# Kernel optimization log

Measured on AMD Instinct MI355X. Metric: run time of the kernel, lower is better.

The kernel has to match this reference:

```python
import jax, jax.numpy as jnp
import numpy as np


def _gcn_prep(edge_index, num_nodes):
    # GCNConv default: remove nothing, add self loops, symmetric normalization
    self_loops = jnp.arange(num_nodes, dtype=edge_index.dtype)
    row = jnp.concatenate([edge_index[0], self_loops])  # source j
    col = jnp.concatenate([edge_index[1], self_loops])  # target i
    deg = jax.ops.segment_sum(jnp.ones_like(col, dtype=jnp.float32), col,
                              num_segments=num_nodes)
    dinv = jnp.where(deg > 0, jax.lax.rsqrt(deg), 0.0)
    norm = dinv[row] * dinv[col]  # [E + N]
    return row, col, norm


def _gcn_conv(x, row, col, norm, W, b):
    # linear transform first (smaller feature dim kept), then gather-scale-scatter
    h = x @ W                               # [N, out]
    msg = h[row] * norm[:, None]            # [E+N, out] gather (irregular access)
    out = jax.ops.segment_sum(msg, col, num_segments=x.shape[0])
    return out + b


def setup_inputs() -> dict:
    key = jax.random.key(0)
    k1, k2, k3, k4, k5 = jax.random.split(key, 5)
    N, F, H, C, E = 50000, 128, 128, 64, 800000
    x = jax.random.normal(k1, (N, F), dtype=jnp.float32)
    edge_index = jax.random.randint(k2, (2, E), 0, N, dtype=jnp.int64)
    # Glorot-ish initialized GCN layer parameters
    W1 = jax.random.normal(k3, (F, H), dtype=jnp.float32) * (1.0 / np.sqrt(F))
    b1 = jnp.zeros((H,), dtype=jnp.float32)
    W2 = jax.random.normal(k4, (H, C), dtype=jnp.float32) * (1.0 / np.sqrt(H))
    b2 = jnp.zeros((C,), dtype=jnp.float32)
    return {"x": x, "edge_index": edge_index, "W1": W1, "b1": b1,
            "W2": W2, "b2": b2}


def reference(x, edge_index, W1, b1, W2, b2):
    # eval-mode forward: dropout(p=0 / eval) is identity
    N = x.shape[0]
    row, col, norm = _gcn_prep(edge_index, N)
    h = _gcn_conv(x, row, col, norm, W1, b1)   # conv1
    h = jax.nn.elu(h)                          # F.elu
    out = _gcn_conv(h, row, col, norm, W2, b2) # conv2
    return out
```

## Files before the change

### kernel.cpp

```cpp
#include <hip/hip_runtime.h>
#include <hip/hip_bf16.h>
#include <math.h>


typedef short bf16x8 __attribute__((ext_vector_type(8)));
typedef float f32x4  __attribute__((ext_vector_type(4)));

#define BCAP 6144
#define CCAP 64

__device__ __forceinline__ unsigned short bf16rne(float f) {
    unsigned u = __float_as_uint(f);
    unsigned r = u + 0x7FFFu + ((u >> 16) & 1u);
    return (unsigned short)(r >> 16);
}
__device__ __forceinline__ float bf16tof(unsigned short h) {
    return __uint_as_float(((unsigned)h) << 16);
}
__device__ __forceinline__ void split2(float v, unsigned short& hi, unsigned short& lo) {
    hi = bf16rne(v);
    lo = bf16rne(v - bf16tof(hi));
}
__device__ __forceinline__ float lo16f(unsigned u) { return __uint_as_float(u << 16); }
__device__ __forceinline__ float hi16f(unsigned u) { return __uint_as_float(u & 0xFFFF0000u); }

__device__ __forceinline__ f32x4 mfma_bf16(bf16x8 a, bf16x8 b, f32x4 c) {
    return __builtin_amdgcn_mfma_f32_16x16x32_bf16(a, b, c, 0, 0, 0);
}

__device__ __forceinline__ int detect64(const int* __restrict__ ei) {
    return (ei[1] | ei[3] | ei[5] | ei[7] | ei[9] | ei[11] | ei[13] | ei[15]) == 0;
}
__device__ __forceinline__ int edge_row(const int* ei, long long E, int is64, int e) {
    return is64 ? ei[2 * (long long)e] : ei[e];
}
__device__ __forceinline__ int edge_col(const int* ei, long long E, int is64, int e) {
    return is64 ? ei[2 * (E + (long long)e)] : ei[E + e];
}

__global__ __launch_bounds__(256) void k_cvt(const float* __restrict__ x,
                                             unsigned short* __restrict__ xhi,
                                             unsigned short* __restrict__ xlo, int total4,
                                             const float* __restrict__ W1,
                                             const float* __restrict__ W2,
                                             unsigned short* __restrict__ w1hi,
                                             unsigned short* __restrict__ w1lo,
                                             unsigned short* __restrict__ w2hi,
                                             unsigned short* __restrict__ w2lo,
                                             int n1, int n2, int H, int C, int nbCvtX) {
    int bid = blockIdx.x;
    if (bid < nbCvtX) {
        int t = bid * 256 + threadIdx.x;
        if (t >= total4) return;
        float4 v = reinterpret_cast<const float4*>(x)[t];
        unsigned short h0, h1, h2, h3, l0, l1, l2, l3;
        split2(v.x, h0, l0); split2(v.y, h1, l1);
        split2(v.z, h2, l2); split2(v.w, h3, l3);
        unsigned long long hp = (unsigned long long)h0 | ((unsigned long long)h1 << 16) |
                                ((unsigned long long)h2 << 32) | ((unsigned long long)h3 << 48);
        unsigned long long lp = (unsigned long long)l0 | ((unsigned long long)l1 << 16) |
                                ((unsigned long long)l2 << 32) | ((unsigned long long)l3 << 48);
        reinterpret_cast<unsigned long long*>(xhi)[t] = hp;
        reinterpret_cast<unsigned long long*>(xlo)[t] = lp;
        return;
    }
    bid -= nbCvtX;
    int t = bid * 256 + threadIdx.x;
    unsigned short h, l;
    if (t < n1) {
        int k = t / H, n = t % H;
        split2(W1[t], h, l);
        w1hi[n * 128 + k] = h;
        w1lo[n * 128 + k] = l;
    } else if (t < n1 + n2) {
        int q = t - n1;
        int k = q / C, n = q % C;
        split2(W2[q], h, l);
        w2hi[n * 128 + k] = h;
        w2lo[n * 128 + k] = l;
    }
}

__global__ __launch_bounds__(256) void k_bucket(const int* __restrict__ ei, int E,
                                                int* __restrict__ bcur,
                                                unsigned* __restrict__ ebuf, int N) {
    __shared__ int lcnt[256];
    __shared__ int lbase[256];
    int t = threadIdx.x;
    lcnt[t] = 0;
    __syncthreads();
    int is64 = detect64(ei);
    int e0 = blockIdx.x * 2048;
    int loff[8], bb[8];
    unsigned pk[8];
    bool val[8];
    #pragma unroll
    for (int k = 0; k < 8; ++k) {
        int e = e0 + k * 256 + t;
        val[k] = (e < E);
        int c = val[k] ? edge_col(ei, E, is64, e) : 0;
        int r = val[k] ? edge_row(ei, E, is64, e) : 0;
        bb[k] = c >> 8;
        pk[k] = ((unsigned)r << 16) | (unsigned)(c & 255);
        loff[k] = val[k] ? atomicAdd(&lcnt[bb[k]], 1) : 0;
    }
    __syncthreads();
    int nbk = (N + 255) >> 8;
    if (t < nbk && lcnt[t] > 0) lbase[t] = atomicAdd(&bcur[t], lcnt[t]);
    __syncthreads();
    #pragma unroll
    for (int k = 0; k < 8; ++k) {
        if (!val[k]) continue;
        int p = lbase[bb[k]] + loff[k];
        if (p < BCAP) ebuf[(size_t)bb[k] * BCAP + p] = pk[k];
    }
}

__global__ __launch_bounds__(256) void k_fine(const unsigned* __restrict__ ebuf,
                                              const int* __restrict__ bcur,
                                              unsigned short* __restrict__ csrc,
                                              int* __restrict__ cnt,
                                              float* __restrict__ dinv, int N) {
    __shared__ int cur[256];
    __shared__ unsigned short slots[256 * CCAP];
    int t = threadIdx.x;
    cur[t] = 0;
    __syncthreads();
    int b = blockIdx.x;
    int cb = bcur[b];
    cb = (cb < BCAP) ? cb : BCAP;
    const unsigned* src = ebuf + (size_t)b * BCAP;
    for (int i = t; i < cb; i += 256) {
        unsigned v = src[i];
        int local = v & 255;
        int pos = atomicAdd(&cur[local], 1);
        if (pos < CCAP) slots[(local << 6) + pos] = (unsigned short)(v >> 16);
    }
    __syncthreads();
    int n0 = b << 8;
    int n = n0 + t;
    if (n < N) {
        int c = cur[t];
        cnt[n] = (c < CCAP) ? c : CCAP;
        dinv[n] = 1.0f / sqrtf((float)(c + 1));
    }
    const unsigned* s32 = reinterpret_cast<const unsigned*>(slots);
    unsigned* d32 = reinterpret_cast<unsigned*>(csrc);
    #pragma unroll
    for (int r = 0; r < 32; ++r) {
        int idx = r * 256 + t;
        int node = idx >> 5, m = idx & 31;
        int gn = n0 + node;
        if (gn < N) d32[(size_t)gn * 32 + m] = s32[(node << 5) + m];
    }
}

template <int NOUT>
__global__ __launch_bounds__(256) void k_gemm_mfma(const unsigned short* __restrict__ Ahi,
                                                   const unsigned short* __restrict__ Alo,
                                                   const unsigned short* __restrict__ BThi,
                                                   const unsigned short* __restrict__ BTlo,
                                                   const float* __restrict__ dinv,
                                                   unsigned short* __restrict__ Cb, int N) {
    constexpr int NT = NOUT / 16;
    int wid = threadIdx.x >> 6, lane = threadIdx.x & 63;
    int row0 = blockIdx.x * 128 + wid * 32;
    int ml = lane & 15, kg = lane >> 4;

    f32x4 acc[2][NT] = {};

    int r0 = row0 + ml, r1 = row0 + 16 + ml;
    int ar0 = (r0 < N) ? r0 : (N - 1);
    int ar1 = (r1 < N) ? r1 : (N - 1);

    for (int kt = 0; kt < 4; ++kt) {
        int k0 = kt * 32 + kg * 8;
        bf16x8 a0h = *reinterpret_cast<const bf16x8*>(&Ahi[(size_t)ar0 * 128 + k0]);
        bf16x8 a0l = *reinterpret_cast<const bf16x8*>(&Alo[(size_t)ar0 * 128 + k0]);
        bf16x8 a1h = *reinterpret_cast<const bf16x8*>(&Ahi[(size_t)ar1 * 128 + k0]);
        bf16x8 a1l = *reinterpret_cast<const bf16x8*>(&Alo[(size_t)ar1 * 128 + k0]);
        #pragma unroll
        for (int nt = 0; nt < NT; ++nt) {
            bf16x8 bh = *reinterpret_cast<const bf16x8*>(&BThi[(size_t)(nt * 16 + ml) * 128 + k0]);
            bf16x8 bl = *reinterpret_cast<const bf16x8*>(&BTlo[(size_t)(nt * 16 + ml) * 128 + k0]);
            acc[0][nt] = mfma_bf16(a0h, bh, acc[0][nt]);
            acc[0][nt] = mfma_bf16(a0l, bh, acc[0][nt]);
            acc[0][nt] = mfma_bf16(a0h, bl, acc[0][nt]);
            acc[1][nt] = mfma_bf16(a1h, bh, acc[1][nt]);
            acc[1][nt] = mfma_bf16(a1l, bh, acc[1][nt]);
            acc[1][nt] = mfma_bf16(a1h, bl, acc[1][nt]);
        }
    }

    #pragma unroll
    for (int rt = 0; rt < 2; ++rt) {
        #pragma unroll
        for (int r = 0; r < 4; ++r) {
            int row = row0 + rt * 16 + kg * 4 + r;
            if (row < N) {
                float d = dinv[row];
                #pragma unroll
                for (int nt = 0; nt < NT; ++nt)
                    Cb[(size_t)row * NOUT + nt * 16 + ml] = bf16rne(acc[rt][nt][r] * d);
            }
        }
    }
}

__global__ __launch_bounds__(256) void k_agg1(const unsigned* __restrict__ hb,
                                              const unsigned short* __restrict__ csr,
                                              const int* __restrict__ cnt,
                                              const float* __restrict__ dinv,
                                              const float* __restrict__ bias,
                                              unsigned* __restrict__ yhi,
                                              unsigned* __restrict__ ylo, int N) {
    int wid  = (blockIdx.x * 256 + threadIdx.x) >> 6;
    int lane = threadIdx.x & 63;
    if (wid >= N) return;
    int i = wid;
    unsigned us = hb[(size_t)i * 64 + lane];
    float ax0 = lo16f(us), ay0 = hi16f(us);
    float ax1 = 0.f, ay1 = 0.f, ax2 = 0.f, ay2 = 0.f, ax3 = 0.f, ay3 = 0.f;
    float ax4 = 0.f, ay4 = 0.f, ax5 = 0.f, ay5 = 0.f, ax6 = 0.f, ay6 = 0.f;
    float ax7 = 0.f, ay7 = 0.f;
    int c = cnt[i];
    int s = i << 6, e = s + c;
    int p = s;
    for (; p + 8 <= e; p += 8) {
        int j0 = csr[p + 0], j1 = csr[p + 1], j2 = csr[p + 2], j3 = csr[p + 3];
        int j4 = csr[p + 4], j5 = csr[p + 5], j6 = csr[p + 6], j7 = csr[p + 7];
        unsigned u0 = hb[(size_t)j0 * 64 + lane];
        unsigned u1 = hb[(size_t)j1 * 64 + lane];
        unsigned u2 = hb[(size_t)j2 * 64 + lane];
        unsigned u3 = hb[(size_t)j3 * 64 + lane];
        unsigned u4 = hb[(size_t)j4 * 64 + lane];
        unsigned u5 = hb[(size_t)j5 * 64 + lane];
        unsigned u6 = hb[(size_t)j6 * 64 + lane];
        unsigned u7 = hb[(size_t)j7 * 64 + lane];
        ax0 += lo16f(u0); ay0 += hi16f(u0);  ax1 += lo16f(u1); ay1 += hi16f(u1);
        ax2 += lo16f(u2); ay2 += hi16f(u2);  ax3 += lo16f(u3); ay3 += hi16f(u3);
        ax4 += lo16f(u4); ay4 += hi16f(u4);  ax5 += lo16f(u5); ay5 += hi16f(u5);
        ax6 += lo16f(u6); ay6 += hi16f(u6);  ax7 += lo16f(u7); ay7 += hi16f(u7);
    }
    if (p + 4 <= e) {
        int j0 = csr[p + 0], j1 = csr[p + 1], j2 = csr[p + 2], j3 = csr[p + 3];
        unsigned u0 = hb[(size_t)j0 * 64 + lane];
        unsigned u1 = hb[(size_t)j1 * 64 + lane];
        unsigned u2 = hb[(size_t)j2 * 64 + lane];
        unsigned u3 = hb[(size_t)j3 * 64 + lane];
        ax0 += lo16f(u0); ay0 += hi16f(u0);  ax1 += lo16f(u1); ay1 += hi16f(u1);
        ax2 += lo16f(u2); ay2 += hi16f(u2);  ax3 += lo16f(u3); ay3 += hi16f(u3);
        p += 4;
    }
    for (; p < e; ++p) {
        unsigned u = hb[(size_t)csr[p] * 64 + lane];
        ax0 += lo16f(u); ay0 += hi16f(u);
    }
    float sx = (ax0 + ax1) + (ax2 + ax3) + (ax4 + ax5) + (ax6 + ax7);
    float sy = (ay0 + ay1) + (ay2 + ay3) + (ay4 + ay5) + (ay6 + ay7);
    float di = dinv[i];
    float2 bb = reinterpret_cast<const float2*>(bias)[lane];
    float vx = di * sx + bb.x;
    float vy = di * sy + bb.y;
    vx = vx > 0.f ? vx : (expf(vx) - 1.f);
    vy = vy > 0.f ? vy : (expf(vy) - 1.f);
    unsigned short hx, lx, hy, ly;
    split2(vx, hx, lx);
    split2(vy, hy, ly);
    yhi[(size_t)i * 64 + lane] = (unsigned)hx | ((unsigned)hy << 16);
    ylo[(size_t)i * 64 + lane] = (unsigned)lx | ((unsigned)ly << 16);
}

__global__ __launch_bounds__(256) void k_agg2(const unsigned short* __restrict__ hb,
                                              const unsigned short* __restrict__ csr,
                                              const int* __restrict__ cnt,
                                              const float* __restrict__ dinv,
                                              const float* __restrict__ bias,
                                              float* __restrict__ out, int N) {
    int wid  = (blockIdx.x * 256 + threadIdx.x) >> 6;
    int lane = threadIdx.x & 63;
    if (wid >= N) return;
    int i = wid;
    float a0 = bf16tof(hb[(size_t)i * 64 + lane]);
    float a1 = 0.f, a2 = 0.f, a3 = 0.f, a4 = 0.f, a5 = 0.f, a6 = 0.f, a7 = 0.f;
    int c = cnt[i];
    int s = i << 6, e = s + c;
    int p = s;
    for (; p + 8 <= e; p += 8) {
        int j0 = csr[p + 0], j1 = csr[p + 1], j2 = csr[p + 2], j3 = csr[p + 3];
        int j4 = csr[p + 4], j5 = csr[p + 5], j6 = csr[p + 6], j7 = csr[p + 7];
        a0 += bf16tof(hb[(size_t)j0 * 64 + lane]);
        a1 += bf16tof(hb[(size_t)j1 * 64 + lane]);
        a2 += bf16tof(hb[(size_t)j2 * 64 + lane]);
        a3 += bf16tof(hb[(size_t)j3 * 64 + lane]);
        a4 += bf16tof(hb[(size_t)j4 * 64 + lane]);
        a5 += bf16tof(hb[(size_t)j5 * 64 + lane]);
        a6 += bf16tof(hb[(size_t)j6 * 64 + lane]);
        a7 += bf16tof(hb[(size_t)j7 * 64 + lane]);
    }
    if (p + 4 <= e) {
        a0 += bf16tof(hb[(size_t)csr[p + 0] * 64 + lane]);
        a1 += bf16tof(hb[(size_t)csr[p + 1] * 64 + lane]);
        a2 += bf16tof(hb[(size_t)csr[p + 2] * 64 + lane]);
        a3 += bf16tof(hb[(size_t)csr[p + 3] * 64 + lane]);
        p += 4;
    }
    for (; p < e; ++p) a0 += bf16tof(hb[(size_t)csr[p] * 64 + lane]);
    float sum = (a0 + a1) + (a2 + a3) + (a4 + a5) + (a6 + a7);
    out[(size_t)i * 64 + lane] = dinv[i] * sum + bias[lane];
}

extern "C" void kernel_launch(void* const* d_in, const int* in_sizes, int n_in,
                              void* d_out, int out_size, void* d_ws, size_t ws_size,
                              hipStream_t stream) {
    const float* x  = (const float*)d_in[0];
    const int*   ei = (const int*)d_in[1];
    const float* W1 = (const float*)d_in[2];
    const float* b1 = (const float*)d_in[3];
    const float* W2 = (const float*)d_in[4];
    const float* b2 = (const float*)d_in[5];

    const int H = in_sizes[3];
    const int C = in_sizes[5];
    const int F = in_sizes[2] / H;
    const int N = in_sizes[0] / F;
    const int E = in_sizes[1] / 2;
    float* out = (float*)d_out;

    char* w = (char*)d_ws;
    auto alloc = [&](size_t bytes) -> char* {
        char* p = w;
        w += (bytes + 255) & ~(size_t)255;
        return p;
    };
    const int nbB = (N + 255) >> 8;
    int*   bcur  = (int*)alloc((size_t)nbB * sizeof(int));
    int*   cnt   = (int*)alloc((size_t)N * sizeof(int));
    float* dinv  = (float*)alloc((size_t)N * sizeof(float));
    unsigned* ebuf = (unsigned*)alloc((size_t)nbB * BCAP * sizeof(unsigned));
    unsigned short* csrc = (unsigned short*)alloc((size_t)N * CCAP * 2);
    unsigned short* xhi  = (unsigned short*)alloc((size_t)N * F * 2);
    unsigned short* xlo  = (unsigned short*)alloc((size_t)N * F * 2);
    unsigned short* w1hi = (unsigned short*)alloc((size_t)F * H * 2);
    unsigned short* w1lo = (unsigned short*)alloc((size_t)F * H * 2);
    unsigned short* w2hi = (unsigned short*)alloc((size_t)H * C * 2);
    unsigned short* w2lo = (unsigned short*)alloc((size_t)H * C * 2);
    unsigned short* h1b  = (unsigned short*)alloc((size_t)N * H * 2);
    unsigned*       y1hi = (unsigned*)alloc((size_t)N * H * 2);
    unsigned*       y1lo = (unsigned*)alloc((size_t)N * H * 2);
    unsigned short* h2b  = (unsigned short*)alloc((size_t)N * C * 2);

    const int total4  = N * F / 4;
    const int nbCvtX  = (total4 + 255) / 256;
    const int nbCvtW  = (F * H + H * C + 255) / 256;
    const int nbAgg   = (N + 3) / 4;

    hipMemsetAsync(bcur, 0, (size_t)nbB * sizeof(int), stream);
    k_bucket<<<(E + 2047) / 2048, 256, 0, stream>>>(ei, E, bcur, ebuf, N);
    k_fine<<<nbB, 256, 0, stream>>>(ebuf, bcur, csrc, cnt, dinv, N);
    k_cvt<<<nbCvtX + nbCvtW, 256, 0, stream>>>(x, xhi, xlo, total4, W1, W2,
                                               w1hi, w1lo, w2hi, w2lo,
                                               F * H, H * C, H, C, nbCvtX);

    k_gemm_mfma<128><<<(N + 127) / 128, 256, 0, stream>>>(xhi, xlo, w1hi, w1lo, dinv, h1b, N);
    k_agg1<<<nbAgg, 256, 0, stream>>>(
        reinterpret_cast<const unsigned*>(h1b), csrc, cnt, dinv, b1, y1hi, y1lo, N);
    k_gemm_mfma<64><<<(N + 127) / 128, 256, 0, stream>>>(
        (const unsigned short*)y1hi, (const unsigned short*)y1lo, w2hi, w2lo, dinv, h2b, N);
    k_agg2<<<nbAgg, 256, 0, stream>>>(h2b, csrc, cnt, dinv, b2, out, N);
}
```

Measured before the change: 144.2 us.

## Fuse x bf16 splitting into GEMM and store layer-2 input as single bf16

Removes the standalone x conversion pass by splitting fp32 x into bf16 hi/lo inside the first GEMM's operand load, eliminating the hi/lo intermediate buffers. The aggregated ELU output now stores only a single bf16 value, and the second GEMM skips the low-part MFMA. This cuts global memory traffic and MFMA work, at the cost of reduced precision for the second layer's input.

```diff
diff --git a/kernel.cpp b/kernel.cpp
--- a/kernel.cpp
+++ b/kernel.cpp
@@ -38,34 +38,14 @@
     return is64 ? ei[2 * (E + (long long)e)] : ei[E + e];
 }
 
-__global__ __launch_bounds__(256) void k_cvt(const float* __restrict__ x,
-                                             unsigned short* __restrict__ xhi,
-                                             unsigned short* __restrict__ xlo, int total4,
-                                             const float* __restrict__ W1,
-                                             const float* __restrict__ W2,
-                                             unsigned short* __restrict__ w1hi,
-                                             unsigned short* __restrict__ w1lo,
-                                             unsigned short* __restrict__ w2hi,
-                                             unsigned short* __restrict__ w2lo,
-                                             int n1, int n2, int H, int C, int nbCvtX) {
-    int bid = blockIdx.x;
-    if (bid < nbCvtX) {
-        int t = bid * 256 + threadIdx.x;
-        if (t >= total4) return;
-        float4 v = reinterpret_cast<const float4*>(x)[t];
-        unsigned short h0, h1, h2, h3, l0, l1, l2, l3;
-        split2(v.x, h0, l0); split2(v.y, h1, l1);
-        split2(v.z, h2, l2); split2(v.w, h3, l3);
-        unsigned long long hp = (unsigned long long)h0 | ((unsigned long long)h1 << 16) |
-                                ((unsigned long long)h2 << 32) | ((unsigned long long)h3 << 48);
-        unsigned long long lp = (unsigned long long)l0 | ((unsigned long long)l1 << 16) |
-                                ((unsigned long long)l2 << 32) | ((unsigned long long)l3 << 48);
-        reinterpret_cast<unsigned long long*>(xhi)[t] = hp;
-        reinterpret_cast<unsigned long long*>(xlo)[t] = lp;
-        return;
-    }
-    bid -= nbCvtX;
-    int t = bid * 256 + threadIdx.x;
+__global__ __launch_bounds__(256) void k_cvtw(const float* __restrict__ W1,
+                                              const float* __restrict__ W2,
+                                              unsigned short* __restrict__ w1hi,
+                                              unsigned short* __restrict__ w1lo,
+                                              unsigned short* __restrict__ w2hi,
+                                              unsigned short* __restrict__ w2lo,
+                                              int n1, int n2, int H, int C) {
+    int t = blockIdx.x * 256 + threadIdx.x;
     unsigned short h, l;
     if (t < n1) {
         int k = t / H, n = t % H;
@@ -155,9 +135,9 @@
     }
 }
 
-template <int NOUT>
-__global__ __launch_bounds__(256) void k_gemm_mfma(const unsigned short* __restrict__ Ahi,
-                                                   const unsigned short* __restrict__ Alo,
+template <int NOUT, bool AF32>
+__global__ __launch_bounds__(256) void k_gemm_mfma(const float* __restrict__ Af,
+                                                   const unsigned short* __restrict__ Ab,
                                                    const unsigned short* __restrict__ BThi,
                                                    const unsigned short* __restrict__ BTlo,
                                                    const float* __restrict__ dinv,
@@ -175,20 +155,45 @@
 
     for (int kt = 0; kt < 4; ++kt) {
         int k0 = kt * 32 + kg * 8;
-        bf16x8 a0h = *reinterpret_cast<const bf16x8*>(&Ahi[(size_t)ar0 * 128 + k0]);
-        bf16x8 a0l = *reinterpret_cast<const bf16x8*>(&Alo[(size_t)ar0 * 128 + k0]);
-        bf16x8 a1h = *reinterpret_cast<const bf16x8*>(&Ahi[(size_t)ar1 * 128 + k0]);
-        bf16x8 a1l = *reinterpret_cast<const bf16x8*>(&Alo[(size_t)ar1 * 128 + k0]);
+        bf16x8 a0h, a0l, a1h, a1l;
+        if constexpr (AF32) {
+            float4 v0 = *reinterpret_cast<const float4*>(&Af[(size_t)ar0 * 128 + k0]);
+            float4 v1 = *reinterpret_cast<const float4*>(&Af[(size_t)ar0 * 128 + k0 + 4]);
+            float4 v2 = *reinterpret_cast<const float4*>(&Af[(size_t)ar1 * 128 + k0]);
+            float4 v3 = *reinterpret_cast<const float4*>(&Af[(size_t)ar1 * 128 + k0 + 4]);
+            unsigned short h, l;
+            split2(v0.x, h, l); a0h[0] = (short)h; a0l[0] = (short)l;
+            split2(v0.y, h, l); a0h[1] = (short)h; a0l[1] = (short)l;
+            split2(v0.z, h, l); a0h[2] = (short)h; a0l[2] = (short)l;
+            split2(v0.w, h, l); a0h[3] = (short)h; a0l[3] = (short)l;
+            split2(v1.x, h, l); a0h[4] = (short)h; a0l[4] = (short)l;
+            split2(v1.y, h, l); a0h[5] = (short)h; a0l[5] = (short)l;
+            split2(v1.z, h, l); a0h[6] = (short)h; a0l[6] = (short)l;
+            split2(v1.w, h, l); a0h[7] = (short)h; a0l[7] = (short)l;
+            split2(v2.x, h, l); a1h[0] = (short)h; a1l[0] = (short)l;
+            split2(v2.y, h, l); a1h[1] = (short)h; a1l[1] = (short)l;
+            split2(v2.z, h, l); a1h[2] = (short)h; a1l[2] = (short)l;
+            split2(v2.w, h, l); a1h[3] = (short)h; a1l[3] = (short)l;
+            split2(v3.x, h, l); a1h[4] = (short)h; a1l[4] = (short)l;
+            split2(v3.y, h, l); a1h[5] = (short)h; a1l[5] = (short)l;
+            split2(v3.z, h, l); a1h[6] = (short)h; a1l[6] = (short)l;
+            split2(v3.w, h, l); a1h[7] = (short)h; a1l[7] = (short)l;
+        } else {
+            a0h = *reinterpret_cast<const bf16x8*>(&Ab[(size_t)ar0 * 128 + k0]);
+            a1h = *reinterpret_cast<const bf16x8*>(&Ab[(size_t)ar1 * 128 + k0]);
+        }
         #pragma unroll
         for (int nt = 0; nt < NT; ++nt) {
             bf16x8 bh = *reinterpret_cast<const bf16x8*>(&BThi[(size_t)(nt * 16 + ml) * 128 + k0]);
             bf16x8 bl = *reinterpret_cast<const bf16x8*>(&BTlo[(size_t)(nt * 16 + ml) * 128 + k0]);
             acc[0][nt] = mfma_bf16(a0h, bh, acc[0][nt]);
-            acc[0][nt] = mfma_bf16(a0l, bh, acc[0][nt]);
             acc[0][nt] = mfma_bf16(a0h, bl, acc[0][nt]);
             acc[1][nt] = mfma_bf16(a1h, bh, acc[1][nt]);
-            acc[1][nt] = mfma_bf16(a1l, bh, acc[1][nt]);
             acc[1][nt] = mfma_bf16(a1h, bl, acc[1][nt]);
+            if constexpr (AF32) {
+                acc[0][nt] = mfma_bf16(a0l, bh, acc[0][nt]);
+                acc[1][nt] = mfma_bf16(a1l, bh, acc[1][nt]);
+            }
         }
     }
 
@@ -212,8 +217,7 @@
                                               const int* __restrict__ cnt,
                                               const float* __restrict__ dinv,
                                               const float* __restrict__ bias,
-                                              unsigned* __restrict__ yhi,
-                                              unsigned* __restrict__ ylo, int N) {
+                                              unsigned* __restrict__ y1b, int N) {
     int wid  = (blockIdx.x * 256 + threadIdx.x) >> 6;
     int lane = threadIdx.x & 63;
     if (wid >= N) return;
@@ -264,11 +268,7 @@
     float vy = di * sy + bb.y;
     vx = vx > 0.f ? vx : (expf(vx) - 1.f);
     vy = vy > 0.f ? vy : (expf(vy) - 1.f);
-    unsigned short hx, lx, hy, ly;
-    split2(vx, hx, lx);
-    split2(vy, hy, ly);
-    yhi[(size_t)i * 64 + lane] = (unsigned)hx | ((unsigned)hy << 16);
-    ylo[(size_t)i * 64 + lane] = (unsigned)lx | ((unsigned)ly << 16);
+    y1b[(size_t)i * 64 + lane] = (unsigned)bf16rne(vx) | ((unsigned)bf16rne(vy) << 16);
 }
 
 __global__ __launch_bounds__(256) void k_agg2(const unsigned short* __restrict__ hb,
@@ -339,33 +339,27 @@
     float* dinv  = (float*)alloc((size_t)N * sizeof(float));
     unsigned* ebuf = (unsigned*)alloc((size_t)nbB * BCAP * sizeof(unsigned));
     unsigned short* csrc = (unsigned short*)alloc((size_t)N * CCAP * 2);
-    unsigned short* xhi  = (unsigned short*)alloc((size_t)N * F * 2);
-    unsigned short* xlo  = (unsigned short*)alloc((size_t)N * F * 2);
     unsigned short* w1hi = (unsigned short*)alloc((size_t)F * H * 2);
     unsigned short* w1lo = (unsigned short*)alloc((size_t)F * H * 2);
     unsigned short* w2hi = (unsigned short*)alloc((size_t)H * C * 2);
     unsigned short* w2lo = (unsigned short*)alloc((size_t)H * C * 2);
     unsigned short* h1b  = (unsigned short*)alloc((size_t)N * H * 2);
-    unsigned*       y1hi = (unsigned*)alloc((size_t)N * H * 2);
-    unsigned*       y1lo = (unsigned*)alloc((size_t)N * H * 2);
+    unsigned*       y1b  = (unsigned*)alloc((size_t)N * H * 2);
     unsigned short* h2b  = (unsigned short*)alloc((size_t)N * C * 2);
 
-    const int total4  = N * F / 4;
-    const int nbCvtX  = (total4 + 255) / 256;
-    const int nbCvtW  = (F * H + H * C + 255) / 256;
-    const int nbAgg   = (N + 3) / 4;
+    const int nbAgg = (N + 3) / 4;
 
     hipMemsetAsync(bcur, 0, (size_t)nbB * sizeof(int), stream);
     k_bucket<<<(E + 2047) / 2048, 256, 0, stream>>>(ei, E, bcur, ebuf, N);
     k_fine<<<nbB, 256, 0, stream>>>(ebuf, bcur, csrc, cnt, dinv, N);
-    k_cvt<<<nbCvtX + nbCvtW, 256, 0, stream>>>(x, xhi, xlo, total4, W1, W2,
-                                               w1hi, w1lo, w2hi, w2lo,
-                                               F * H, H * C, H, C, nbCvtX);
-
-    k_gemm_mfma<128><<<(N + 127) / 128, 256, 0, stream>>>(xhi, xlo, w1hi, w1lo, dinv, h1b, N);
+    k_cvtw<<<(F * H + H * C + 255) / 256, 256, 0, stream>>>(W1, W2, w1hi, w1lo, w2hi, w2lo,
+                                                            F * H, H * C, H, C);
+
+    k_gemm_mfma<128, true><<<(N + 127) / 128, 256, 0, stream>>>(
+        x, nullptr, w1hi, w1lo, dinv, h1b, N);
     k_agg1<<<nbAgg, 256, 0, stream>>>(
-        reinterpret_cast<const unsigned*>(h1b), csrc, cnt, dinv, b1, y1hi, y1lo, N);
-    k_gemm_mfma<64><<<(N + 127) / 128, 256, 0, stream>>>(
-        (const unsigned short*)y1hi, (const unsigned short*)y1lo, w2hi, w2lo, dinv, h2b, N);
+        reinterpret_cast<const unsigned*>(h1b), csrc, cnt, dinv, b1, y1b, N);
+    k_gemm_mfma<64, false><<<(N + 127) / 128, 256, 0, stream>>>(
+        nullptr, (const unsigned short*)y1b, w2hi, w2lo, dinv, h2b, N);
     k_agg2<<<nbAgg, 256, 0, stream>>>(h2b, csrc, cnt, dinv, b2, out, N);
 }
```

Result: faster. 133.0 us (-7.7%).
